# Performance work log

Hardware: AMD Instinct MI355X
Metric: run time of the kernel (lower is better)

Reference implementation:

```python
import jax, jax.numpy as jnp
import numpy as np

N_NODES = 100000
N_EDGES = 1600000
IN_CH, HID_CH, OUT_CH = 128, 128, 64


def setup_inputs() -> dict:
    key = jax.random.key(0)
    k_x, k_e, k1, k2, k3 = jax.random.split(key, 5)
    x = jax.random.normal(k_x, (N_NODES, IN_CH), dtype=jnp.float32)
    edge_index = jax.random.randint(k_e, (2, N_EDGES), 0, N_NODES, dtype=jnp.int64)
    # Glorot-ish init for the three GCNConv weight matrices (no bias).
    W1 = jax.random.normal(k1, (IN_CH, HID_CH), dtype=jnp.float32) / np.sqrt(IN_CH)
    W2 = jax.random.normal(k2, (HID_CH, HID_CH), dtype=jnp.float32) / np.sqrt(HID_CH)
    W3 = jax.random.normal(k3, (HID_CH, OUT_CH), dtype=jnp.float32) / np.sqrt(HID_CH)
    return {"x": x, "edge_index": edge_index, "W1": W1, "W2": W2, "W3": W3}


def _gcn_layer(x, src, dst, W):
    # GCNConv(normalize=False, bias=False): transform then sum-aggregate over edges.
    h = x @ W                      # [N, d_out]
    msgs = h[src]                  # [E, d_out] gather from source nodes
    return jax.ops.segment_sum(msgs, dst, num_segments=N_NODES)  # scatter-add to targets


def reference(x, edge_index, W1, W2, W3):
    src, dst = edge_index[0], edge_index[1]  # PyG flow: source_to_target
    h = _gcn_layer(x, src, dst, W1)
    h = _gcn_layer(h, src, dst, W2)
    h = _gcn_layer(h, src, dst, W3)
    return h  # [N, OUT_CH]
```

## Files before the change

kernel.cpp:

```cpp
#include <hip/hip_runtime.h>

#define N_NODES 100000
#define N_EDGES 1600000
#define CAP 48
#define NBUCK 256
#define NPB 391
#define SCAP 8192
#define NREP 4
#define SCAP4 (SCAP / NREP)
#define EPB 4096
#define NBIN ((N_EDGES + EPB - 1) / EPB)

typedef unsigned int uint;
typedef unsigned short ushort;

__device__ __forceinline__ void fma4(float4& c, float s, const float4& w) {
    c.x += s * w.x; c.y += s * w.y; c.z += s * w.z; c.w += s * w.w;
}

__device__ __forceinline__ ushort bf16r(float f) {
    union { float f; uint u; } v; v.f = f;
    return (ushort)((v.u + 0x7fffu + ((v.u >> 16) & 1u)) >> 16);
}

struct alignas(16) GemmSmem {
    float Xs[128][36];
    float Ws[32][64];
};

template <typename OutT>
__device__ __forceinline__ void gemm64_block(GemmSmem& sm, int bid,
                                             const float* __restrict__ X,
                                             const float* __restrict__ W,
                                             OutT* __restrict__ H, int n) {
    const int tid  = threadIdx.x;
    const int row0 = bid * 128;
    const int rg   = tid >> 4;
    const int cg   = tid & 15;

    float4 acc0[8];
#pragma unroll
    for (int r = 0; r < 8; r++) acc0[r] = make_float4(0.f, 0.f, 0.f, 0.f);

    const int lr = tid >> 1;
    const int lh = tid & 1;
    int grow = row0 + lr; if (grow > n - 1) grow = n - 1;
    const float* gx_base = X + (size_t)grow * 128 + lh * 16;

    for (int k0 = 0; k0 < 128; k0 += 32) {
        const float* gx = gx_base + k0;
#pragma unroll
        for (int i = 0; i < 4; i++)
            *(float4*)&sm.Xs[lr][lh * 16 + 4 * i] = *(const float4*)(gx + 4 * i);
        const float4* gw = (const float4*)(W + (size_t)k0 * 64);
        float4* sw = (float4*)&sm.Ws[0][0];
#pragma unroll
        for (int i = 0; i < 2; i++) sw[tid + 256 * i] = gw[tid + 256 * i];
        __syncthreads();

#pragma unroll
        for (int kk = 0; kk < 32; kk += 4) {
            float4 w00 = *(const float4*)&sm.Ws[kk + 0][cg * 4];
            float4 w01 = *(const float4*)&sm.Ws[kk + 1][cg * 4];
            float4 w02 = *(const float4*)&sm.Ws[kk + 2][cg * 4];
            float4 w03 = *(const float4*)&sm.Ws[kk + 3][cg * 4];
#pragma unroll
            for (int r = 0; r < 8; r++) {
                float4 a = *(const float4*)&sm.Xs[rg + 16 * r][kk];
                fma4(acc0[r], a.x, w00);
                fma4(acc0[r], a.y, w01);
                fma4(acc0[r], a.z, w02);
                fma4(acc0[r], a.w, w03);
            }
        }
        __syncthreads();
    }

#pragma unroll
    for (int r = 0; r < 8; r++) {
        int row = row0 + rg + 16 * r;
        if (row < n) {
            if constexpr (sizeof(OutT) == 2) {
                ushort4 o0 = make_ushort4(bf16r(acc0[r].x), bf16r(acc0[r].y),
                                          bf16r(acc0[r].z), bf16r(acc0[r].w));
                *(ushort4*)&H[(size_t)row * 64 + cg * 4] = o0;
            } else {
                *(float4*)&H[(size_t)row * 64 + cg * 4] = *(float4*)&acc0[r];
            }
        }
    }
}

union BinWcSmem {
    struct {
        int ecnt[NBUCK];
        int base[NBUCK];
        int lofs[NBUCK];
        uint2 estage[EPB];
    } b;
    GemmSmem g;
};

__global__ void __launch_bounds__(256) bin_wc(const int* __restrict__ src,
                                              const int* __restrict__ dst,
                                              int* __restrict__ gcur,
                                              uint2* __restrict__ seg, int E,
                                              const float* __restrict__ W1,
                                              const float* __restrict__ W2,
                                              const float* __restrict__ W3,
                                              float* __restrict__ W23,
                                              float* __restrict__ Wc) {
    __shared__ BinWcSmem sh;
    if (blockIdx.x == gridDim.x - 1) {
        gemm64_block<float>(sh.g, 0, W2, W3, W23, 128);
        __syncthreads();
        gemm64_block<float>(sh.g, 0, W1, W23, Wc, 128);
        return;
    }
    const int t = threadIdx.x;
    sh.b.ecnt[t] = 0;
    __syncthreads();
    const int e0 = blockIdx.x * EPB;
    const int rep = blockIdx.x & (NREP - 1);
    uint sreg[EPB / 256];
    int  dreg[EPB / 256];
    int  slreg[EPB / 256];
#pragma unroll
    for (int k = 0; k < EPB / 256; k++) {
        int i = e0 + k * 256 + t;
        if (i < E) {
            int d = dst[i];
            sreg[k] = (uint)src[i];
            dreg[k] = d;
            slreg[k] = atomicAdd(&sh.b.ecnt[d / NPB], 1);
        }
    }
    __syncthreads();
    const int c = sh.b.ecnt[t];
    sh.b.base[t] = (c > 0) ? atomicAdd(&gcur[rep * NBUCK + t], c) : 0;
    sh.b.lofs[t] = c;
    __syncthreads();
#pragma unroll
    for (int off = 1; off < NBUCK; off <<= 1) {
        int u = (t >= off) ? sh.b.lofs[t - off] : 0;
        __syncthreads();
        sh.b.lofs[t] += u;
        __syncthreads();
    }
    const int excl = sh.b.lofs[t] - c;
    __syncthreads();
    sh.b.lofs[t] = excl;
    __syncthreads();
#pragma unroll
    for (int k = 0; k < EPB / 256; k++) {
        int i = e0 + k * 256 + t;
        if (i < E) {
            int b = dreg[k] / NPB;
            sh.b.estage[sh.b.lofs[b] + slreg[k]] =
                make_uint2(sreg[k], (uint)dreg[k]);
        }
    }
    __syncthreads();
    const int total = min(E - e0, EPB);
    for (int i = t; i < total; i += 256) {
        uint2 e = sh.b.estage[i];
        int b = (int)e.y / NPB;
        int s = sh.b.base[b] + (i - sh.b.lofs[b]);
        if (s < SCAP4)
            seg[(size_t)b * SCAP + rep * SCAP4 + s] = e;
    }
}

union CsrGemmSmem {
    struct {
        int lc[NPB];
        int lrp[NPB];
        int sc[2][512];
    } c;
    GemmSmem g;
};

__global__ void __launch_bounds__(256, 3) csr_gemm(const int* __restrict__ gcur,
                                                   const uint2* __restrict__ seg,
                                                   int* __restrict__ col,
                                                   int* __restrict__ cnt,
                                                   int* __restrict__ rowptr,
                                                   const float* __restrict__ X,
                                                   const float* __restrict__ Wc,
                                                   ushort* __restrict__ Y, int n) {
    __shared__ CsrGemmSmem sh;
    if (blockIdx.x < NBUCK) {
        const int b = blockIdx.x;
        const int t = threadIdx.x;
        const int node0 = b * NPB;
        for (int i = t; i < NPB; i += 256) sh.c.lc[i] = 0;
        __syncthreads();
#pragma unroll
        for (int q = 0; q < NREP; q++) {
            int m = gcur[q * NBUCK + b]; if (m > SCAP4) m = SCAP4;
            const uint2* sg = seg + (size_t)b * SCAP + q * SCAP4;
            for (int i = t; i < m; i += 256)
                atomicAdd(&sh.c.lc[(int)sg[i].y - node0], 1);
        }
        __syncthreads();
        sh.c.sc[0][t]       = (t < NPB) ? ((sh.c.lc[t] + 3) & ~3) : 0;
        sh.c.sc[0][t + 256] = (t + 256 < NPB) ? ((sh.c.lc[t + 256] + 3) & ~3) : 0;
        __syncthreads();
        int pb = 0;
#pragma unroll
        for (int off = 1; off < 512; off <<= 1) {
            int a0 = sh.c.sc[pb][t];
            int a1 = sh.c.sc[pb][t + 256];
            int b0 = (t >= off) ? sh.c.sc[pb][t - off] : 0;
            int b1 = (t + 256 >= off) ? sh.c.sc[pb][t + 256 - off] : 0;
            sh.c.sc[pb ^ 1][t]       = a0 + b0;
            sh.c.sc[pb ^ 1][t + 256] = a1 + b1;
            __syncthreads();
            pb ^= 1;
        }
        if (t < NPB)
            sh.c.lrp[t] = sh.c.sc[pb][t] - ((sh.c.lc[t] + 3) & ~3);
        if (t + 256 < NPB)
            sh.c.lrp[t + 256] = sh.c.sc[pb][t + 256] - ((sh.c.lc[t + 256] + 3) & ~3);
        __syncthreads();
        for (int i = t; i < NPB; i += 256) sh.c.lc[i] = 0;
        __syncthreads();
#pragma unroll
        for (int q = 0; q < NREP; q++) {
            int m = gcur[q * NBUCK + b]; if (m > SCAP4) m = SCAP4;
            const uint2* sg = seg + (size_t)b * SCAP + q * SCAP4;
            for (int i = t; i < m; i += 256) {
                uint2 e = sg[i];
                int dn = (int)e.y - node0;
                int slot = atomicAdd(&sh.c.lc[dn], 1);
                int pos = sh.c.lrp[dn] + slot;
                if (pos < SCAP) col[(size_t)b * SCAP + pos] = (int)e.x;
            }
        }
        __syncthreads();
        for (int i = t; i < NPB; i += 256) {
            int node = node0 + i;
            if (node < n) {
                int c = sh.c.lc[i];
                cnt[node] = (c > CAP) ? CAP : c;
                rowptr[node] = b * SCAP + sh.c.lrp[i];
            }
        }
    } else {
        gemm64_block<ushort>(sh.g, blockIdx.x - NBUCK, X, Wc, Y, n);
    }
}

__device__ __forceinline__ float2 bf2f(uint u) {
    union { uint u; float f; } a, b;
    a.u = u << 16; b.u = u & 0xffff0000u;
    return make_float2(a.f, b.f);
}

template <bool FINAL>
__global__ void __launch_bounds__(256) agg64(const uint4* __restrict__ T_in,
                                             const int* __restrict__ cnt,
                                             const int* __restrict__ col,
                                             const int* __restrict__ rowptr,
                                             void* __restrict__ T_out, int n) {
    int gid  = blockIdx.x * blockDim.x + threadIdx.x;
    int node = gid >> 3;
    int lane = gid & 7;
    if (node >= n) return;
    int m = cnt[node]; if (m > CAP) m = CAP;
    const int* cb = col + rowptr[node];
    const uint4* tb = T_in + lane;
    float4 accA = make_float4(0.f, 0.f, 0.f, 0.f);
    float4 accB = make_float4(0.f, 0.f, 0.f, 0.f);
    int j = 0;
    for (; j + 8 <= m; j += 8) {
        int4 c0 = *(const int4*)&cb[j];
        int4 c1 = *(const int4*)&cb[j + 4];
        uint4 u0 = tb[(size_t)c0.x * 8];
        uint4 u1 = tb[(size_t)c0.y * 8];
        uint4 u2 = tb[(size_t)c0.z * 8];
        uint4 u3 = tb[(size_t)c0.w * 8];
        uint4 u4 = tb[(size_t)c1.x * 8];
        uint4 u5 = tb[(size_t)c1.y * 8];
        uint4 u6 = tb[(size_t)c1.z * 8];
        uint4 u7 = tb[(size_t)c1.w * 8];
        float2 p0 = bf2f(u0.x), p1 = bf2f(u1.x), p2 = bf2f(u2.x), p3 = bf2f(u3.x);
        float2 p4 = bf2f(u4.x), p5 = bf2f(u5.x), p6 = bf2f(u6.x), p7 = bf2f(u7.x);
        accA.x += ((p0.x + p1.x) + (p2.x + p3.x)) + ((p4.x + p5.x) + (p6.x + p7.x));
        accA.y += ((p0.y + p1.y) + (p2.y + p3.y)) + ((p4.y + p5.y) + (p6.y + p7.y));
        float2 q0 = bf2f(u0.y), q1 = bf2f(u1.y), q2 = bf2f(u2.y), q3 = bf2f(u3.y);
        float2 q4 = bf2f(u4.y), q5 = bf2f(u5.y), q6 = bf2f(u6.y), q7 = bf2f(u7.y);
        accA.z += ((q0.x + q1.x) + (q2.x + q3.x)) + ((q4.x + q5.x) + (q6.x + q7.x));
        accA.w += ((q0.y + q1.y) + (q2.y + q3.y)) + ((q4.y + q5.y) + (q6.y + q7.y));
        float2 r0 = bf2f(u0.z), r1 = bf2f(u1.z), r2 = bf2f(u2.z), r3 = bf2f(u3.z);
        float2 r4 = bf2f(u4.z), r5 = bf2f(u5.z), r6 = bf2f(u6.z), r7 = bf2f(u7.z);
        accB.x += ((r0.x + r1.x) + (r2.x + r3.x)) + ((r4.x + r5.x) + (r6.x + r7.x));
        accB.y += ((r0.y + r1.y) + (r2.y + r3.y)) + ((r4.y + r5.y) + (r6.y + r7.y));
        float2 s0 = bf2f(u0.w), s1 = bf2f(u1.w), s2 = bf2f(u2.w), s3 = bf2f(u3.w);
        float2 s4 = bf2f(u4.w), s5 = bf2f(u5.w), s6 = bf2f(u6.w), s7 = bf2f(u7.w);
        accB.z += ((s0.x + s1.x) + (s2.x + s3.x)) + ((s4.x + s5.x) + (s6.x + s7.x));
        accB.w += ((s0.y + s1.y) + (s2.y + s3.y)) + ((s4.y + s5.y) + (s6.y + s7.y));
    }
    for (; j + 4 <= m; j += 4) {
        int4 c0 = *(const int4*)&cb[j];
        uint4 u0 = tb[(size_t)c0.x * 8];
        uint4 u1 = tb[(size_t)c0.y * 8];
        uint4 u2 = tb[(size_t)c0.z * 8];
        uint4 u3 = tb[(size_t)c0.w * 8];
        float2 p0 = bf2f(u0.x), p1 = bf2f(u1.x), p2 = bf2f(u2.x), p3 = bf2f(u3.x);
        accA.x += (p0.x + p1.x) + (p2.x + p3.x);
        accA.y += (p0.y + p1.y) + (p2.y + p3.y);
        float2 q0 = bf2f(u0.y), q1 = bf2f(u1.y), q2 = bf2f(u2.y), q3 = bf2f(u3.y);
        accA.z += (q0.x + q1.x) + (q2.x + q3.x);
        accA.w += (q0.y + q1.y) + (q2.y + q3.y);
        float2 r0 = bf2f(u0.z), r1 = bf2f(u1.z), r2 = bf2f(u2.z), r3 = bf2f(u3.z);
        accB.x += (r0.x + r1.x) + (r2.x + r3.x);
        accB.y += (r0.y + r1.y) + (r2.y + r3.y);
        float2 s0 = bf2f(u0.w), s1 = bf2f(u1.w), s2 = bf2f(u2.w), s3 = bf2f(u3.w);
        accB.z += (s0.x + s1.x) + (s2.x + s3.x);
        accB.w += (s0.y + s1.y) + (s2.y + s3.y);
    }
    for (; j < m; j++) {
        uint4 u = tb[(size_t)cb[j] * 8];
        float2 p = bf2f(u.x), q = bf2f(u.y), r = bf2f(u.z), s = bf2f(u.w);
        accA.x += p.x; accA.y += p.y; accA.z += q.x; accA.w += q.y;
        accB.x += r.x; accB.y += r.y; accB.z += s.x; accB.w += s.y;
    }
    if (FINAL) {
        ((float4*)T_out)[(size_t)node * 16 + lane * 2]     = accA;
        ((float4*)T_out)[(size_t)node * 16 + lane * 2 + 1] = accB;
    } else {
        uint4 o;
        o.x = (uint)bf16r(accA.x) | ((uint)bf16r(accA.y) << 16);
        o.y = (uint)bf16r(accA.z) | ((uint)bf16r(accA.w) << 16);
        o.z = (uint)bf16r(accB.x) | ((uint)bf16r(accB.y) << 16);
        o.w = (uint)bf16r(accB.z) | ((uint)bf16r(accB.w) << 16);
        ((uint4*)T_out)[(size_t)node * 8 + lane] = o;
    }
}


static inline size_t align_up(size_t x, size_t a) { return (x + a - 1) & ~(a - 1); }

extern "C" void kernel_launch(void* const* d_in, const int* in_sizes, int n_in,
                              void* d_out, int out_size, void* d_ws, size_t ws_size,
                              hipStream_t stream) {
    const float* x  = (const float*)d_in[0];
    const int*   ei = (const int*)d_in[1];
    const float* W1 = (const float*)d_in[2];
    const float* W2 = (const float*)d_in[3];
    const float* W3 = (const float*)d_in[4];
    float* out = (float*)d_out;

    const int N = N_NODES;
    const int E = N_EDGES;
    const int* src = ei;
    const int* dst = ei + E;

    char* p = (char*)d_ws;
    int*    gcur   = (int*)p;   p += align_up((size_t)NREP * NBUCK * 4, 256);
    int*    cnt    = (int*)p;   p += align_up((size_t)N * 4, 256);
    int*    rowptr = (int*)p;   p += align_up((size_t)N * 4, 256);
    uint2*  seg    = (uint2*)p; p += align_up((size_t)NBUCK * SCAP * 8, 256);
    int*    col    = (int*)p;   p += align_up((size_t)NBUCK * SCAP * 4, 256);
    float*  W23    = (float*)p; p += align_up((size_t)128 * 64 * 4, 256);
    float*  Wc     = (float*)p; p += align_up((size_t)128 * 64 * 4, 256);
    ushort* Y      = (ushort*)p; p += align_up((size_t)N * 64 * 2, 256);
    ushort* Za     = (ushort*)p; p += align_up((size_t)N * 64 * 2, 256);

    hipMemsetAsync(gcur, 0, (size_t)NREP * NBUCK * 4, stream);

    bin_wc<<<NBIN + 1, 256, 0, stream>>>(src, dst, gcur, seg, E,
                                         W1, W2, W3, W23, Wc);

    const int gemm_blocks = (N + 127) / 128;
    csr_gemm<<<NBUCK + gemm_blocks, 256, 0, stream>>>(gcur, seg, col, cnt,
                                                      rowptr, x, Wc, Y, N);

    const int agg_blocks = (N * 8 + 255) / 256;
    agg64<false><<<agg_blocks, 256, 0, stream>>>((const uint4*)Y,  cnt, col,
                                                 rowptr, Za, N);
    agg64<false><<<agg_blocks, 256, 0, stream>>>((const uint4*)Za, cnt, col,
                                                 rowptr, Y,  N);
    agg64<true ><<<agg_blocks, 256, 0, stream>>>((const uint4*)Y,  cnt, col,
                                                 rowptr, out, N);
}
```

Before: 242.9 us.

## Pack binned edges into 32-bit words and use wave-shuffle bucket scan

Each binned edge is now packed into one 32-bit word: the source index shifted left by 9 bits, with the local destination offset in the low 9 bits. This halves the intermediate seg buffer traffic written by bin_wc and read twice by csr_gemm, and shrinks the shared staging array. The block-wide Hillis-Steele scan over bucket counts is replaced by a wave64 shuffle scan plus per-wave sums, which removes many barriers. Packing limits source ids to 23 bits, which 100000 nodes fit, and adds a byte array to carry the bucket id through staging.

```diff
diff --git a/kernel.cpp b/kernel.cpp
--- a/kernel.cpp
+++ b/kernel.cpp
@@ -13,6 +13,7 @@
 
 typedef unsigned int uint;
 typedef unsigned short ushort;
+typedef unsigned char uchar;
 
 __device__ __forceinline__ void fma4(float4& c, float s, const float4& w) {
     c.x += s * w.x; c.y += s * w.y; c.z += s * w.z; c.w += s * w.w;
@@ -96,7 +97,9 @@
         int ecnt[NBUCK];
         int base[NBUCK];
         int lofs[NBUCK];
-        uint2 estage[EPB];
+        int wsum[4];
+        uint  estage[EPB];
+        uchar eb[EPB];
     } b;
     GemmSmem g;
 };
@@ -104,7 +107,7 @@
 __global__ void __launch_bounds__(256) bin_wc(const int* __restrict__ src,
                                               const int* __restrict__ dst,
                                               int* __restrict__ gcur,
-                                              uint2* __restrict__ seg, int E,
+                                              uint* __restrict__ seg, int E,
                                               const float* __restrict__ W1,
                                               const float* __restrict__ W2,
                                               const float* __restrict__ W3,
@@ -122,52 +125,54 @@
     __syncthreads();
     const int e0 = blockIdx.x * EPB;
     const int rep = blockIdx.x & (NREP - 1);
-    uint sreg[EPB / 256];
-    int  dreg[EPB / 256];
-    int  slreg[EPB / 256];
+    uint preg[EPB / 256];
+    uint qreg[EPB / 256];
 #pragma unroll
     for (int k = 0; k < EPB / 256; k++) {
         int i = e0 + k * 256 + t;
         if (i < E) {
             int d = dst[i];
-            sreg[k] = (uint)src[i];
-            dreg[k] = d;
-            slreg[k] = atomicAdd(&sh.b.ecnt[d / NPB], 1);
+            int b = d / NPB;
+            preg[k] = ((uint)src[i] << 9) | (uint)(d - b * NPB);
+            int slot = atomicAdd(&sh.b.ecnt[b], 1);
+            qreg[k] = ((uint)b << 12) | (uint)slot;
         }
     }
     __syncthreads();
     const int c = sh.b.ecnt[t];
     sh.b.base[t] = (c > 0) ? atomicAdd(&gcur[rep * NBUCK + t], c) : 0;
-    sh.b.lofs[t] = c;
-    __syncthreads();
-#pragma unroll
-    for (int off = 1; off < NBUCK; off <<= 1) {
-        int u = (t >= off) ? sh.b.lofs[t - off] : 0;
-        __syncthreads();
-        sh.b.lofs[t] += u;
-        __syncthreads();
-    }
-    const int excl = sh.b.lofs[t] - c;
-    __syncthreads();
+    int v = c;
+#pragma unroll
+    for (int off = 1; off < 64; off <<= 1) {
+        int u = __shfl_up(v, off, 64);
+        if ((t & 63) >= off) v += u;
+    }
+    if ((t & 63) == 63) sh.b.wsum[t >> 6] = v;
+    __syncthreads();
+    int woff = 0;
+#pragma unroll
+    for (int w = 0; w < 4; w++) if (w < (t >> 6)) woff += sh.b.wsum[w];
+    const int excl = woff + v - c;
     sh.b.lofs[t] = excl;
     __syncthreads();
 #pragma unroll
     for (int k = 0; k < EPB / 256; k++) {
         int i = e0 + k * 256 + t;
         if (i < E) {
-            int b = dreg[k] / NPB;
-            sh.b.estage[sh.b.lofs[b] + slreg[k]] =
-                make_uint2(sreg[k], (uint)dreg[k]);
+            int b = (int)(qreg[k] >> 12);
+            int pos = sh.b.lofs[b] + (int)(qreg[k] & 4095u);
+            sh.b.estage[pos] = preg[k];
+            sh.b.eb[pos] = (uchar)b;
         }
     }
     __syncthreads();
     const int total = min(E - e0, EPB);
     for (int i = t; i < total; i += 256) {
-        uint2 e = sh.b.estage[i];
-        int b = (int)e.y / NPB;
+        uint w = sh.b.estage[i];
+        int b = (int)sh.b.eb[i];
         int s = sh.b.base[b] + (i - sh.b.lofs[b]);
         if (s < SCAP4)
-            seg[(size_t)b * SCAP + rep * SCAP4 + s] = e;
+            seg[(size_t)b * SCAP + rep * SCAP4 + s] = w;
     }
 }
 
@@ -181,7 +186,7 @@
 };
 
 __global__ void __launch_bounds__(256, 3) csr_gemm(const int* __restrict__ gcur,
-                                                   const uint2* __restrict__ seg,
+                                                   const uint* __restrict__ seg,
                                                    int* __restrict__ col,
                                                    int* __restrict__ cnt,
                                                    int* __restrict__ rowptr,
@@ -198,9 +203,9 @@
 #pragma unroll
         for (int q = 0; q < NREP; q++) {
             int m = gcur[q * NBUCK + b]; if (m > SCAP4) m = SCAP4;
-            const uint2* sg = seg + (size_t)b * SCAP + q * SCAP4;
+            const uint* sg = seg + (size_t)b * SCAP + q * SCAP4;
             for (int i = t; i < m; i += 256)
-                atomicAdd(&sh.c.lc[(int)sg[i].y - node0], 1);
+                atomicAdd(&sh.c.lc[(int)(sg[i] & 511u)], 1);
         }
         __syncthreads();
         sh.c.sc[0][t]       = (t < NPB) ? ((sh.c.lc[t] + 3) & ~3) : 0;
@@ -228,13 +233,13 @@
 #pragma unroll
         for (int q = 0; q < NREP; q++) {
             int m = gcur[q * NBUCK + b]; if (m > SCAP4) m = SCAP4;
-            const uint2* sg = seg + (size_t)b * SCAP + q * SCAP4;
+            const uint* sg = seg + (size_t)b * SCAP + q * SCAP4;
             for (int i = t; i < m; i += 256) {
-                uint2 e = sg[i];
-                int dn = (int)e.y - node0;
+                uint w = sg[i];
+                int dn = (int)(w & 511u);
                 int slot = atomicAdd(&sh.c.lc[dn], 1);
                 int pos = sh.c.lrp[dn] + slot;
-                if (pos < SCAP) col[(size_t)b * SCAP + pos] = (int)e.x;
+                if (pos < SCAP) col[(size_t)b * SCAP + pos] = (int)(w >> 9);
             }
         }
         __syncthreads();
@@ -361,7 +366,7 @@
     int*    gcur   = (int*)p;   p += align_up((size_t)NREP * NBUCK * 4, 256);
     int*    cnt    = (int*)p;   p += align_up((size_t)N * 4, 256);
     int*    rowptr = (int*)p;   p += align_up((size_t)N * 4, 256);
-    uint2*  seg    = (uint2*)p; p += align_up((size_t)NBUCK * SCAP * 8, 256);
+    uint*   seg    = (uint*)p;  p += align_up((size_t)NBUCK * SCAP * 4, 256);
     int*    col    = (int*)p;   p += align_up((size_t)NBUCK * SCAP * 4, 256);
     float*  W23    = (float*)p; p += align_up((size_t)128 * 64 * 4, 256);
     float*  Wc     = (float*)p; p += align_up((size_t)128 * 64 * 4, 256);
```

After: 241.8 us. About the same (-0.5%).
